# Optimization experiments

Hardware: AMD Instinct MI355X
Metric: run time of the kernel (lower is better)

## Reference

```python
import jax, jax.numpy as jnp
import numpy as np
import math

# config constants (match init_kwargs)
H = 1024; NH = 16; NKV = 4; HD = 64; E = 16; I = 512
NG = 4; TKG = 2; TK = 4; ROUTED_SCALE = 2.5; EPS = 1e-6; THETA = 10000.0
B = 2; S = 1024


def setup_inputs() -> dict:
    key = jax.random.key(0)
    ks = jax.random.split(key, 16)
    sd = 0.02
    inp = {
        "hidden_states": jax.random.normal(ks[0], (B, S, H), jnp.float32),
        "position_ids": jnp.arange(B * S, dtype=jnp.int64).reshape(B, S) % 4096,
        "ln1_w": jnp.ones((H,), jnp.float32),
        "ln2_w": jnp.ones((H,), jnp.float32),
        "q_w": jax.random.normal(ks[1], (NH * HD, H), jnp.float32) * sd,
        "k_w": jax.random.normal(ks[2], (NKV * HD, H), jnp.float32) * sd,
        "v_w": jax.random.normal(ks[3], (NKV * HD, H), jnp.float32) * sd,
        "o_w": jax.random.normal(ks[4], (H, NH * HD), jnp.float32) * sd,
        "gate_w": jax.random.normal(ks[5], (E, H), jnp.float32) * sd,
        "e_bias": jax.random.normal(ks[6], (E,), jnp.float32) * 0.1,
        "W_gu": jax.random.normal(ks[7], (E, 2 * I, H), jnp.float32) * sd,
        "W_d": jax.random.normal(ks[8], (E, H, I), jnp.float32) * sd,
        "sg_w": jax.random.normal(ks[9], (2 * I, H), jnp.float32) * sd,
        "su_w": jax.random.normal(ks[10], (2 * I, H), jnp.float32) * sd,
        "sd_w": jax.random.normal(ks[11], (H, 2 * I), jnp.float32) * sd,
    }
    return inp


def _rmsnorm(x, w, eps=EPS):
    v = jnp.mean(x.astype(jnp.float32) ** 2, axis=-1, keepdims=True)
    return w * (x * jax.lax.rsqrt(v + eps)).astype(w.dtype)


def _rotate_half(x):
    x1, x2 = x[..., : HD // 2], x[..., HD // 2 :]
    return jnp.concatenate([-x2, x1], axis=-1)


def _attention(hs, position_ids, q_w, k_w, v_w, o_w):
    b, s, _ = hs.shape
    q = (hs @ q_w.T).reshape(b, s, NH, HD).transpose(0, 2, 1, 3)   # [B,NH,S,HD]
    k = (hs @ k_w.T).reshape(b, s, NKV, HD).transpose(0, 2, 1, 3)
    v = (hs @ v_w.T).reshape(b, s, NKV, HD).transpose(0, 2, 1, 3)
    # RoPE
    inv_freq = 1.0 / (THETA ** (jnp.arange(0, HD, 2, dtype=jnp.float32) / HD))
    freqs = position_ids.astype(jnp.float32)[..., None] * inv_freq  # [B,S,HD/2]
    emb = jnp.concatenate([freqs, freqs], axis=-1)                  # [B,S,HD]
    cos = jnp.cos(emb)[:, None]                                     # [B,1,S,HD]
    sin = jnp.sin(emb)[:, None]
    q = q * cos + _rotate_half(q) * sin
    k = k * cos + _rotate_half(k) * sin
    # GQA: repeat kv heads
    groups = NH // NKV
    k = jnp.repeat(k, groups, axis=1)
    v = jnp.repeat(v, groups, axis=1)
    scale = 1.0 / math.sqrt(HD)
    scores = jnp.einsum("bhsd,bhtd->bhst", q, k) * scale
    causal = jnp.triu(jnp.full((s, s), -jnp.inf, jnp.float32), k=1)
    scores = scores + causal[None, None]
    attn = jax.nn.softmax(scores.astype(jnp.float32), axis=-1).astype(q.dtype)
    out = jnp.einsum("bhst,bhtd->bhsd", attn, v)
    out = out.transpose(0, 2, 1, 3).reshape(b, s, NH * HD)
    return out @ o_w.T


def _moe(x, gate_w, e_bias, W_gu, W_d, sg_w, su_w, sd_w):
    b, s, h = x.shape
    xf = x.reshape(-1, h)                                     # [T,H]
    T = xf.shape[0]
    logits = xf.astype(jnp.float32) @ gate_w.astype(jnp.float32).T  # [T,E]
    scores = jax.nn.sigmoid(logits)
    sfc = scores + e_bias[None]
    # group-restricted top-k
    gsize = E // NG
    group_scores = sfc.reshape(T, NG, gsize).max(axis=-1)     # [T,NG]
    _, gidx = jax.lax.top_k(group_scores, TKG)                # [T,TKG]
    gmask = jnp.zeros((T, NG), bool).at[jnp.arange(T)[:, None], gidx].set(True)
    smask = jnp.repeat(gmask, gsize, axis=1)                  # [T,E]
    masked = jnp.where(smask, sfc, 0.0)
    _, topk_idx = jax.lax.top_k(masked, TK)                   # [T,TK]
    topk_w = jnp.take_along_axis(scores, topk_idx, axis=1)    # [T,TK]
    topk_w = topk_w / (topk_w.sum(axis=-1, keepdims=True) + 1e-20)
    topk_w = (topk_w * ROUTED_SCALE).astype(xf.dtype)
    # combine weights [T,E] (scatter-add over selected experts)
    combine = jnp.zeros((T, E), xf.dtype).at[
        jnp.arange(T)[:, None], topk_idx].add(topk_w)
    # dense expert compute (static shapes), weighted combine fused in einsum
    gu = jnp.einsum("th,eih->tei", xf, W_gu)                  # [T,E,2I]
    hidden = jax.nn.silu(gu[..., :I]) * gu[..., I:]           # [T,E,I]
    routed = jnp.einsum("tei,ehi,te->th", hidden, W_d, combine)
    # shared experts
    shared = ((jax.nn.silu(xf @ sg_w.T) * (xf @ su_w.T)) @ sd_w.T)
    return (routed + shared).reshape(b, s, h)


def reference(hidden_states, position_ids, ln1_w, ln2_w, q_w, k_w, v_w, o_w,
              gate_w, e_bias, W_gu, W_d, sg_w, su_w, sd_w):
    res = hidden_states
    hs = _rmsnorm(hidden_states, ln1_w)
    hs = res + _attention(hs, position_ids, q_w, k_w, v_w, o_w)
    res = hs
    hs = _rmsnorm(hs, ln2_w)
    hs = res + _moe(hs, gate_w, e_bias, W_gu, W_d, sg_w, su_w, sd_w)
    return hs
```

## Files before the change

### kernel.cpp

```cpp
#include <hip/hip_runtime.h>
#include <hip/hip_bf16.h>
#include <stdint.h>

typedef float f32x4 __attribute__((ext_vector_type(4)));
typedef short s16x8 __attribute__((ext_vector_type(8)));
typedef short s16x4 __attribute__((ext_vector_type(4)));

__device__ __forceinline__ short f2bf(float x) {
    union { float f; uint32_t u; } v; v.f = x;
    uint32_t r = v.u + 0x7fffu + ((v.u >> 16) & 1u);
    return (short)(r >> 16);
}
__device__ __forceinline__ float bf2f(short b) {
    union { uint32_t u; float f; } v; v.u = ((uint32_t)(uint16_t)b) << 16;
    return v.f;
}
__device__ __forceinline__ void gld16(const void* g, void* l) {
    __builtin_amdgcn_global_load_lds((const __attribute__((address_space(1))) uint32_t*)g,
                                     (__attribute__((address_space(3))) uint32_t*)l, 16, 0, 0);
}

__global__ __launch_bounds__(256) void cvt_all_kernel(const float* __restrict__ q, const float* __restrict__ k,
                                                      const float* __restrict__ v, const float* __restrict__ o,
                                                      const float* __restrict__ gu, const float* __restrict__ wd,
                                                      const float* __restrict__ sg, const float* __restrict__ su,
                                                      const float* __restrict__ sd, short* __restrict__ wqkv,
                                                      short* __restrict__ wo, short* __restrict__ wgu,
                                                      short* __restrict__ wdB, short* __restrict__ wsgsu,
                                                      short* __restrict__ wsd) {
    const size_t total = 3866624;
    size_t stride = (size_t)gridDim.x * 256;
    for (size_t i = (size_t)blockIdx.x * 256 + threadIdx.x; i < total; i += stride) {
        const float* src; short* dst;
        if (i < 327680) {
            if (i < 131072) { src = q + i * 8; dst = wqkv + i * 8; }
            else if (i < 163840) { src = k + (i - 131072) * 8; dst = wqkv + 1048576 + (i - 131072) * 8; }
            else if (i < 196608) { src = v + (i - 163840) * 8; dst = wqkv + 1310720 + (i - 163840) * 8; }
            else { src = o + (i - 196608) * 8; dst = wo + (i - 196608) * 8; }
        } else if (i < 3473408) {
            if (i < 2424832) { src = gu + (i - 327680) * 8; dst = wgu + (i - 327680) * 8; }
            else { src = wd + (i - 2424832) * 8; dst = wdB + (i - 2424832) * 8; }
        } else {
            if (i < 3604480) { src = sg + (i - 3473408) * 8; dst = wsgsu + (i - 3473408) * 8; }
            else if (i < 3735552) { src = su + (i - 3604480) * 8; dst = wsgsu + 1048576 + (i - 3604480) * 8; }
            else { src = sd + (i - 3735552) * 8; dst = wsd + (i - 3735552) * 8; }
        }
        f32x4 a = ((const f32x4*)src)[0];
        f32x4 b = ((const f32x4*)src)[1];
        s16x8 o8;
        o8[0] = f2bf(a[0]); o8[1] = f2bf(a[1]); o8[2] = f2bf(a[2]); o8[3] = f2bf(a[3]);
        o8[4] = f2bf(b[0]); o8[5] = f2bf(b[1]); o8[6] = f2bf(b[2]); o8[7] = f2bf(b[3]);
        *(s16x8*)dst = o8;
    }
}

__global__ __launch_bounds__(256) void rmsnorm_kernel(const float* __restrict__ x, const float* __restrict__ w,
                                                      short* __restrict__ out) {
    int t = blockIdx.x;
    f32x4 v = ((const f32x4*)(x + (size_t)t * 1024))[threadIdx.x];
    float ssq = v[0]*v[0] + v[1]*v[1] + v[2]*v[2] + v[3]*v[3];
#pragma unroll
    for (int o = 1; o < 64; o <<= 1) ssq += __shfl_xor(ssq, o);
    __shared__ float red[4];
    if ((threadIdx.x & 63) == 0) red[threadIdx.x >> 6] = ssq;
    __syncthreads();
    float tot = red[0] + red[1] + red[2] + red[3];
    float rs = rsqrtf(tot * (1.0f / 1024.0f) + 1e-6f);
    f32x4 wv = ((const f32x4*)w)[threadIdx.x];
    s16x4 o4;
#pragma unroll
    for (int j = 0; j < 4; ++j) o4[j] = f2bf(v[j] * rs * wv[j]);
    ((s16x4*)(out + (size_t)t * 1024))[threadIdx.x] = o4;
}

__global__ __launch_bounds__(256) void addnorm_kernel(const float* __restrict__ a, const float* __restrict__ b,
                                                      const float* __restrict__ w, float* __restrict__ res,
                                                      short* __restrict__ xf, float* __restrict__ xf32) {
    int t = blockIdx.x;
    f32x4 va = ((const f32x4*)(a + (size_t)t * 1024))[threadIdx.x];
    f32x4 vb = ((const f32x4*)(b + (size_t)t * 1024))[threadIdx.x]
             + ((const f32x4*)(b + (size_t)2048 * 1024 + (size_t)t * 1024))[threadIdx.x];
    f32x4 s = va + vb;
    ((f32x4*)(res + (size_t)t * 1024))[threadIdx.x] = s;
    float ssq = s[0]*s[0] + s[1]*s[1] + s[2]*s[2] + s[3]*s[3];
#pragma unroll
    for (int o = 1; o < 64; o <<= 1) ssq += __shfl_xor(ssq, o);
    __shared__ float red[4];
    if ((threadIdx.x & 63) == 0) red[threadIdx.x >> 6] = ssq;
    __syncthreads();
    float tot = red[0] + red[1] + red[2] + red[3];
    float rs = rsqrtf(tot * (1.0f / 1024.0f) + 1e-6f);
    f32x4 wv = ((const f32x4*)w)[threadIdx.x];
    f32x4 xo;
    s16x4 o4;
#pragma unroll
    for (int j = 0; j < 4; ++j) { xo[j] = s[j] * rs * wv[j]; o4[j] = f2bf(xo[j]); }
    ((f32x4*)(xf32 + (size_t)t * 1024))[threadIdx.x] = xo;
    ((s16x4*)(xf + (size_t)t * 1024))[threadIdx.x] = o4;
}

__global__ __launch_bounds__(256, 4) void gemm2_kernel(const short* __restrict__ A, const short* __restrict__ Bg,
                                                       void* __restrict__ Cv, int M, int N, int Ktot, int Ksub,
                                                       const int* __restrict__ counts, const int* __restrict__ lists,
                                                       const int* __restrict__ plan, int a_shift, int store_bf16) {
    __shared__ short As[2][128 * 32];
    __shared__ short Bs[2][128 * 32];
    int e, bm, bn, k0, Mloc;
    size_t coff;
    const int* rl = nullptr;
    if (plan) {
        int wi = blockIdx.y;
        if (wi >= plan[0]) return;
        int it = plan[1 + wi];
        e = it & 31; bm = (it >> 5) * 128;
        bn = blockIdx.x * 128; k0 = 0;
        Mloc = counts[e]; rl = lists + e * 2048; coff = 0;
    } else {
        e = 0; bm = blockIdx.x * 128; bn = blockIdx.y * 128;
        k0 = blockIdx.z * Ksub; Mloc = M;
        coff = (size_t)blockIdx.z * M * N;
    }
    if (bm >= Mloc) return;
    const short* Bt = Bg + (size_t)e * N * Ktot;
    int tid = threadIdx.x, w = tid >> 6, l = tid & 63;
    int lr = l & 15, lg = l >> 4;
    int rsub = l >> 2, u = l & 3;
    int fs = (rsub & 3) ^ ((rsub >> 2) & 3);
    int colsel = (u ^ fs) * 8;
    int ra = w * 32 + rsub;
    int ga0 = bm + ra;       if (ga0 > Mloc - 1) ga0 = Mloc - 1;
    int ga1 = bm + ra + 16;  if (ga1 > Mloc - 1) ga1 = Mloc - 1;
    int ar0 = rl ? (rl[ga0] >> a_shift) : ga0;
    int ar1 = rl ? (rl[ga1] >> a_shift) : ga1;
    const short* Ap0 = A + (size_t)ar0 * Ktot + k0 + colsel;
    const short* Ap1 = A + (size_t)ar1 * Ktot + k0 + colsel;
    const short* Bp0 = Bt + (size_t)(bn + ra) * Ktot + k0 + colsel;
    const short* Bp1 = Bt + (size_t)(bn + ra + 16) * Ktot + k0 + colsel;
    int lb0 = w * 1024, lb1 = w * 1024 + 512;

    int wm = (w >> 1) * 64, wn = (w & 1) * 64;
    int su = lg ^ (lr & 3) ^ ((lr >> 2) & 3);
    int aoff[4], boff[4];
#pragma unroll
    for (int mf = 0; mf < 4; ++mf) aoff[mf] = (wm + mf * 16 + lr) * 32 + su * 8;
#pragma unroll
    for (int nf = 0; nf < 4; ++nf) boff[nf] = (wn + nf * 16 + lr) * 32 + su * 8;

    f32x4 zero4 = {0.f, 0.f, 0.f, 0.f};
    f32x4 acc[4][4];
#pragma unroll
    for (int mf = 0; mf < 4; ++mf)
#pragma unroll
        for (int nf = 0; nf < 4; ++nf) acc[mf][nf] = zero4;

#define STAGE(buf, kt) do { \
        gld16(Ap0 + (kt) * 32, &As[buf][lb0]); \
        gld16(Ap1 + (kt) * 32, &As[buf][lb1]); \
        gld16(Bp0 + (kt) * 32, &Bs[buf][lb0]); \
        gld16(Bp1 + (kt) * 32, &Bs[buf][lb1]); \
    } while (0)

    int nk = Ksub >> 5;
    STAGE(0, 0);
    asm volatile("s_waitcnt vmcnt(0)");
    __syncthreads();
    for (int kt = 0; kt < nk; ++kt) {
        int cur = kt & 1;
        if (kt + 1 < nk) STAGE(cur ^ 1, kt + 1);
        s16x8 af[4], bfr[4];
#pragma unroll
        for (int mf = 0; mf < 4; ++mf) af[mf] = *(const s16x8*)&As[cur][aoff[mf]];
#pragma unroll
        for (int nf = 0; nf < 4; ++nf) bfr[nf] = *(const s16x8*)&Bs[cur][boff[nf]];
#pragma unroll
        for (int mf = 0; mf < 4; ++mf)
#pragma unroll
            for (int nf = 0; nf < 4; ++nf)
                acc[mf][nf] = __builtin_amdgcn_mfma_f32_16x16x32_bf16(af[mf], bfr[nf], acc[mf][nf], 0, 0, 0);
        __syncthreads();
    }
#undef STAGE
    float* Cf = (float*)Cv;
    short* Cs = (short*)Cv;
#pragma unroll
    for (int mf = 0; mf < 4; ++mf) {
        int rbase = bm + wm + mf * 16 + lg * 4;
#pragma unroll
        for (int r = 0; r < 4; ++r) {
            int grow = rbase + r;
            if (grow < Mloc) {
                int crow = rl ? rl[grow] : grow;
                size_t cb = coff + (size_t)crow * N + bn + wn + lr;
                if (store_bf16) {
#pragma unroll
                    for (int nf = 0; nf < 4; ++nf) Cs[cb + nf * 16] = f2bf(acc[mf][nf][r]);
                } else {
#pragma unroll
                    for (int nf = 0; nf < 4; ++nf) Cf[cb + nf * 16] = acc[mf][nf][r];
                }
            }
        }
    }
}

__global__ __launch_bounds__(64) void rope_kernel(const float* __restrict__ qkv, short* __restrict__ Qr,
                                                  short* __restrict__ Kr, short* __restrict__ Vt) {
    int t = blockIdx.x;
    int b = t >> 10, s = t & 1023;
    int l = threadIdx.x;
    __shared__ float cs[32], sn[32], qrow[1024], krow[256], vrow[256];
    const f32x4* r0 = (const f32x4*)(qkv + (size_t)t * 1536);
    const f32x4* r1 = (const f32x4*)(qkv + (size_t)2048 * 1536 + (size_t)t * 1536);
#pragma unroll
    for (int i = 0; i < 4; ++i) ((f32x4*)qrow)[l + i * 64] = r0[l + i * 64] + r1[l + i * 64];
    ((f32x4*)krow)[l] = r0[256 + l] + r1[256 + l];
    ((f32x4*)vrow)[l] = r0[320 + l] + r1[320 + l];
    if (l < 32) {
        float fr = (float)t * exp2f(-(float)l * 0.41524101186f);
        cs[l] = cosf(fr); sn[l] = sinf(fr);
    }
    __syncthreads();
    int d = l;
    float c = cs[d & 31], sv = sn[d & 31];
#pragma unroll
    for (int h = 0; h < 16; ++h) {
        float x = qrow[h * 64 + d];
        float rot = (d < 32) ? -qrow[h * 64 + d + 32] : qrow[h * 64 + d - 32];
        Qr[((size_t)(b * 16 + h) * 1024 + s) * 64 + d] = f2bf((x * c + rot * sv) * 0.125f);
    }
#pragma unroll
    for (int h = 0; h < 4; ++h) {
        float x = krow[h * 64 + d];
        float rot = (d < 32) ? -krow[h * 64 + d + 32] : krow[h * 64 + d - 32];
        Kr[((size_t)(b * 4 + h) * 1024 + s) * 64 + d] = f2bf(x * c + rot * sv);
        Vt[((size_t)(b * 4 + h) * 64 + d) * 1024 + s] = f2bf(vrow[h * 64 + d]);
    }
}

struct KV { s16x8 k[4]; s16x8 v[4]; };
__device__ __forceinline__ void kv_load(KV& r, const short* Kb, const short* Vb, int k0, int lr, int lg) {
    const short* K0 = Kb + (size_t)(k0 + lr) * 64 + lg * 8;
    const short* K1 = Kb + (size_t)(k0 + 16 + lr) * 64 + lg * 8;
    r.k[0] = *(const s16x8*)K0;
    r.k[1] = *(const s16x8*)(K0 + 32);
    r.k[2] = *(const s16x8*)K1;
    r.k[3] = *(const s16x8*)(K1 + 32);
#pragma unroll
    for (int dt = 0; dt < 4; ++dt)
        r.v[dt] = *(const s16x8*)(Vb + (size_t)(dt * 16 + lr) * 1024 + k0 + lg * 8);
}
__device__ __forceinline__ void chain_step(const KV& kv, s16x8 qf0, s16x8 qf1, f32x4* o,
                                           float& m, float& lsum, short* Pl,
                                           int lr, int lg, int k0, int qmask) {
    f32x4 z = {0.f, 0.f, 0.f, 0.f};
    f32x4 sc0 = z, sc1 = z;
    sc0 = __builtin_amdgcn_mfma_f32_16x16x32_bf16(kv.k[0], qf0, sc0, 0, 0, 0);
    sc0 = __builtin_amdgcn_mfma_f32_16x16x32_bf16(kv.k[1], qf1, sc0, 0, 0, 0);
    sc1 = __builtin_amdgcn_mfma_f32_16x16x32_bf16(kv.k[2], qf0, sc1, 0, 0, 0);
    sc1 = __builtin_amdgcn_mfma_f32_16x16x32_bf16(kv.k[3], qf1, sc1, 0, 0, 0);
#pragma unroll
    for (int r = 0; r < 4; ++r) {
        if (k0 + lg * 4 + r > qmask) sc0[r] = -1e30f;
        if (k0 + 16 + lg * 4 + r > qmask) sc1[r] = -1e30f;
    }
    float tm = fmaxf(fmaxf(fmaxf(sc0[0], sc0[1]), fmaxf(sc0[2], sc0[3])),
                     fmaxf(fmaxf(sc1[0], sc1[1]), fmaxf(sc1[2], sc1[3])));
    tm = fmaxf(tm, __shfl_xor(tm, 16));
    tm = fmaxf(tm, __shfl_xor(tm, 32));
    float newm = fmaxf(m, tm);
    float fac = __expf(m - newm);
    float p[8];
#pragma unroll
    for (int r = 0; r < 4; ++r) { p[r] = __expf(sc0[r] - newm); p[4 + r] = __expf(sc1[r] - newm); }
    float ts = ((p[0] + p[1]) + (p[2] + p[3])) + ((p[4] + p[5]) + (p[6] + p[7]));
    ts += __shfl_xor(ts, 16);
    ts += __shfl_xor(ts, 32);
    lsum = lsum * fac + ts;
    m = newm;
    s16x4 w0, w1;
#pragma unroll
    for (int r = 0; r < 4; ++r) { w0[r] = f2bf(p[r]); w1[r] = f2bf(p[4 + r]); }
    *(s16x4*)&Pl[lr * 40 + lg * 4] = w0;
    *(s16x4*)&Pl[lr * 40 + 16 + lg * 4] = w1;
    s16x8 pf = *(const s16x8*)&Pl[lr * 40 + lg * 8];
#pragma unroll
    for (int dt = 0; dt < 4; ++dt) {
        o[dt] *= fac;
        o[dt] = __builtin_amdgcn_mfma_f32_16x16x32_bf16(kv.v[dt], pf, o[dt], 0, 0, 0);
    }
}

__global__ __launch_bounds__(64) void attn_kernel(const short* __restrict__ Qr, const short* __restrict__ Kr,
                                                  const short* __restrict__ Vt, short* __restrict__ attn_out) {
    int p = blockIdx.x;
    int hb = blockIdx.y;
    int b = hb >> 4, h = hb & 15, kv = h >> 2;
    int l = threadIdx.x;
    int lr = l & 15, lg = l >> 4;
    int q0A = p * 16, q0B = (63 - p) * 16;
    __shared__ short PlA[16 * 40], PlB[16 * 40];
    const short* Qh = Qr + (size_t)(b * 16 + h) * 1024 * 64;
    s16x8 qA0 = *(const s16x8*)(Qh + (size_t)(q0A + lr) * 64 + lg * 8);
    s16x8 qA1 = *(const s16x8*)(Qh + (size_t)(q0A + lr) * 64 + 32 + lg * 8);
    s16x8 qB0 = *(const s16x8*)(Qh + (size_t)(q0B + lr) * 64 + lg * 8);
    s16x8 qB1 = *(const s16x8*)(Qh + (size_t)(q0B + lr) * 64 + 32 + lg * 8);
    const short* Kbase = Kr + (size_t)(b * 4 + kv) * 1024 * 64;
    const short* Vbase = Vt + (size_t)(b * 4 + kv) * 64 * 1024;

    f32x4 zero4 = {0.f, 0.f, 0.f, 0.f};
    f32x4 oA[4], oB[4];
#pragma unroll
    for (int dt = 0; dt < 4; ++dt) { oA[dt] = zero4; oB[dt] = zero4; }
    float mA = -1e30f, lsA = 0.f, mB = -1e30f, lsB = 0.f;
    int ntA = (q0A + 47) >> 5, ntB = (q0B + 47) >> 5;
    int qmA = q0A + lr, qmB = q0B + lr;
    const int BIG = 1 << 29;

    KV b0, b1;
    kv_load(b0, Kbase, Vbase, 0, lr, lg);
    for (int kt = 0; kt < ntB; kt += 2) {
        if (kt + 1 < ntB) kv_load(b1, Kbase, Vbase, (kt + 1) * 32, lr, lg);
        if (kt < ntA) chain_step(b0, qA0, qA1, oA, mA, lsA, PlA, lr, lg, kt * 32,
                                 (kt == ntA - 1) ? qmA : BIG);
        chain_step(b0, qB0, qB1, oB, mB, lsB, PlB, lr, lg, kt * 32,
                   (kt == ntB - 1) ? qmB : BIG);
        if (kt + 1 >= ntB) break;
        if (kt + 2 < ntB) kv_load(b0, Kbase, Vbase, (kt + 2) * 32, lr, lg);
        if (kt + 1 < ntA) chain_step(b1, qA0, qA1, oA, mA, lsA, PlA, lr, lg, (kt + 1) * 32,
                                     (kt + 1 == ntA - 1) ? qmA : BIG);
        chain_step(b1, qB0, qB1, oB, mB, lsB, PlB, lr, lg, (kt + 1) * 32,
                   (kt + 1 == ntB - 1) ? qmB : BIG);
    }
    float invA = 1.f / lsA, invB = 1.f / lsB;
    short* oa = attn_out + ((size_t)(b * 1024 + q0A + lr)) * 1024 + h * 64;
    short* ob = attn_out + ((size_t)(b * 1024 + q0B + lr)) * 1024 + h * 64;
#pragma unroll
    for (int dt = 0; dt < 4; ++dt)
#pragma unroll
        for (int r = 0; r < 4; ++r) {
            oa[dt * 16 + lg * 4 + r] = f2bf(oA[dt][r] * invA);
            ob[dt * 16 + lg * 4 + r] = f2bf(oB[dt][r] * invB);
        }
}

__global__ __launch_bounds__(256) void router_topk_kernel(const float* __restrict__ x32, const float* __restrict__ gw,
                                                          const float* __restrict__ eb, float* __restrict__ tw,
                                                          int* __restrict__ tidx) {
    int t = blockIdx.x * 4 + (threadIdx.x >> 6);
    int l = threadIdx.x & 63;
    const float* x = x32 + (size_t)t * 1024;
    f32x4 xv[4];
#pragma unroll
    for (int j = 0; j < 4; ++j) xv[j] = *(const f32x4*)(x + j * 256 + l * 4);
    float acc[16];
#pragma unroll
    for (int e = 0; e < 16; ++e) {
        float a = 0.f;
#pragma unroll
        for (int j = 0; j < 4; ++j) {
            f32x4 g = *(const f32x4*)(gw + (size_t)e * 1024 + j * 256 + l * 4);
            a += xv[j][0]*g[0] + xv[j][1]*g[1] + xv[j][2]*g[2] + xv[j][3]*g[3];
        }
        acc[e] = a;
    }
#pragma unroll
    for (int e = 0; e < 16; ++e) {
#pragma unroll
        for (int o = 1; o < 64; o <<= 1) acc[e] += __shfl_xor(acc[e], o);
    }
    if (l == 0) {
        float score[16], sfc[16];
#pragma unroll
        for (int e = 0; e < 16; ++e) {
            score[e] = 1.f / (1.f + __expf(-acc[e]));
            sfc[e] = score[e] + eb[e];
        }
        float gs[4];
#pragma unroll
        for (int g = 0; g < 4; ++g)
            gs[g] = fmaxf(fmaxf(sfc[4 * g], sfc[4 * g + 1]), fmaxf(sfc[4 * g + 2], sfc[4 * g + 3]));
        int g1 = 0;
        for (int g = 1; g < 4; ++g) if (gs[g] > gs[g1]) g1 = g;
        int g2 = -1;
        for (int g = 0; g < 4; ++g) {
            if (g == g1) continue;
            if (g2 < 0 || gs[g] > gs[g2]) g2 = g;
        }
        float masked[16];
#pragma unroll
        for (int e = 0; e < 16; ++e) {
            int g = e >> 2;
            masked[e] = (g == g1 || g == g2) ? sfc[e] : 0.0f;
        }
        float tot = 1e-20f;
        int idx[4]; float wv[4];
        for (int k = 0; k < 4; ++k) {
            int bi = 0;
            float bv = -1e30f;
            for (int e2 = 0; e2 < 16; ++e2)
                if (masked[e2] > bv) { bv = masked[e2]; bi = e2; }
            idx[k] = bi;
            wv[k] = score[bi];
            masked[bi] = -1e30f;
            tot += wv[k];
        }
        for (int k = 0; k < 4; ++k) {
            tw[t * 4 + k] = wv[k] / tot * 2.5f;
            tidx[t * 4 + k] = idx[k];
        }
    }
}

__global__ __launch_bounds__(64) void router_lists_kernel(const int* __restrict__ tidx, int* __restrict__ counts,
                                                          int* __restrict__ lists) {
    int e = blockIdx.x;
    int l = threadIdx.x;
    int base = 0;
    for (int it = 0; it < 128; ++it) {
        int p = it * 64 + l;
        bool match = (tidx[p] == e);
        unsigned long long mask = __ballot(match);
        int pos = __popcll(mask & ((1ull << l) - 1ull));
        if (match) lists[e * 2048 + base + pos] = p;
        base += __popcll(mask);
    }
    if (l == 0) counts[e] = base;
}

__global__ void plan_kernel(const int* __restrict__ counts, int* __restrict__ plan) {
    if (threadIdx.x == 0) {
        int n = 0;
        for (int e = 0; e < 16; ++e) {
            int nb = (counts[e] + 127) >> 7;
            for (int m2 = 0; m2 < nb; ++m2) plan[1 + n++] = e | (m2 << 5);
        }
        plan[0] = n;
    }
}

__global__ __launch_bounds__(128) void silu_routed_kernel(const short* __restrict__ gu, short* __restrict__ hid) {
    int pr = blockIdx.x;
    int j = threadIdx.x * 4;
    s16x4 gv = *(const s16x4*)(gu + (size_t)pr * 1024 + j);
    s16x4 uv = *(const s16x4*)(gu + (size_t)pr * 1024 + 512 + j);
    s16x4 o;
#pragma unroll
    for (int k = 0; k < 4; ++k) {
        float gf = bf2f(gv[k]);
        o[k] = f2bf(gf / (1.f + __expf(-gf)) * bf2f(uv[k]));
    }
    *(s16x4*)(hid + (size_t)pr * 512 + j) = o;
}

__global__ __launch_bounds__(256) void silu_shared_kernel(const short* __restrict__ gu, short* __restrict__ h) {
    int t = blockIdx.x;
    int j = threadIdx.x * 4;
    s16x4 gv = *(const s16x4*)(gu + (size_t)t * 2048 + j);
    s16x4 uv = *(const s16x4*)(gu + (size_t)t * 2048 + 1024 + j);
    s16x4 o;
#pragma unroll
    for (int k = 0; k < 4; ++k) {
        float gf = bf2f(gv[k]);
        o[k] = f2bf(gf / (1.f + __expf(-gf)) * bf2f(uv[k]));
    }
    *(s16x4*)(h + (size_t)t * 1024 + j) = o;
}

__global__ __launch_bounds__(256) void combine_kernel(const float* __restrict__ res2, const float* __restrict__ sdp,
                                                      const short* __restrict__ slots, const float* __restrict__ tw,
                                                      float* __restrict__ out) {
    int t = blockIdx.x;
    int i = threadIdx.x;
    f32x4 a = ((const f32x4*)(res2 + (size_t)t * 1024))[i];
    f32x4 s0 = ((const f32x4*)(sdp + (size_t)t * 1024))[i];
    f32x4 s1 = ((const f32x4*)(sdp + (size_t)2048 * 1024 + (size_t)t * 1024))[i];
    f32x4 acc = a + s0 + s1;
#pragma unroll
    for (int s = 0; s < 4; ++s) {
        float w = tw[t * 4 + s];
        s16x4 d = ((const s16x4*)(slots + (size_t)(t * 4 + s) * 1024))[i];
#pragma unroll
        for (int j = 0; j < 4; ++j) acc[j] += bf2f(d[j]) * w;
    }
    ((f32x4*)(out + (size_t)t * 1024))[i] = acc;
}

extern "C" void kernel_launch(void* const* d_in, const int* in_sizes, int n_in,
                              void* d_out, int out_size, void* d_ws, size_t ws_size,
                              hipStream_t stream) {
    const float* hidden = (const float*)d_in[0];
    const float* ln1 = (const float*)d_in[2];
    const float* ln2 = (const float*)d_in[3];
    const float* qw = (const float*)d_in[4];
    const float* kw = (const float*)d_in[5];
    const float* vw = (const float*)d_in[6];
    const float* ow = (const float*)d_in[7];
    const float* gatew = (const float*)d_in[8];
    const float* ebias = (const float*)d_in[9];
    const float* wgu = (const float*)d_in[10];
    const float* wd = (const float*)d_in[11];
    const float* sgw = (const float*)d_in[12];
    const float* suw = (const float*)d_in[13];
    const float* sdw = (const float*)d_in[14];
    float* out = (float*)d_out;

    char* base = (char*)d_ws;
    size_t off = 0;
    auto alloc = [&](size_t bytes) -> char* {
        char* r = base + off;
        off += (bytes + 255) & ~(size_t)255;
        return r;
    };
    const size_t MB = 1u << 20;

    short* wqkv_b = (short*)alloc((size_t)1536 * 1024 * 2);
    short* wo_b   = (short*)alloc((size_t)1024 * 1024 * 2);
    short* wgu_b  = (short*)alloc((size_t)16 * 1024 * 1024 * 2);
    short* wd_b   = (short*)alloc((size_t)16 * 1024 * 512 * 2);
    short* wsgsu_b= (short*)alloc((size_t)2048 * 1024 * 2);
    short* wsd_b  = (short*)alloc((size_t)1024 * 1024 * 2);
    float* res2 = (float*)alloc((size_t)2048 * 1024 * 4);
    short* xf   = (short*)alloc((size_t)2048 * 1024 * 2);
    float* topkw = (float*)alloc(2048 * 4 * 4);
    int* tidx   = (int*)alloc(8192 * 4);
    int* counts = (int*)alloc(64);
    int* lists  = (int*)alloc(16 * 2048 * 4);
    int* plan   = (int*)alloc(512);
    short* gu_or_sgsu = (short*)alloc((size_t)8192 * 1024 * 2);
    short* shhid = (short*)alloc((size_t)2048 * 1024 * 2);
    short* hid   = (short*)alloc((size_t)8192 * 512 * 2);

    char* ov = alloc(50 * MB);
    short* xn1       = (short*)(ov);
    float* qkv_part  = (float*)(ov + 4 * MB);
    short* Qr        = (short*)(ov);
    short* Kr        = (short*)(ov + 28 * MB);
    short* Vt        = (short*)(ov + 29 * MB);
    short* attn_out  = (short*)(ov + 30 * MB);
    float* attnproj_part = (float*)(ov + 34 * MB);
    float* xf32      = (float*)(ov);
    short* down_slot = (short*)(ov + 8 * MB);
    float* sd_part   = (float*)(ov + 24 * MB);

    cvt_all_kernel<<<2048, 256, 0, stream>>>(qw, kw, vw, ow, wgu, wd, sgw, suw, sdw,
                                             wqkv_b, wo_b, wgu_b, wd_b, wsgsu_b, wsd_b);

    rmsnorm_kernel<<<2048, 256, 0, stream>>>(hidden, ln1, xn1);
    gemm2_kernel<<<dim3(16, 12, 2), 256, 0, stream>>>(xn1, wqkv_b, qkv_part, 2048, 1536, 1024, 512,
                                                      nullptr, nullptr, nullptr, 0, 0);
    rope_kernel<<<2048, 64, 0, stream>>>(qkv_part, Qr, Kr, Vt);
    attn_kernel<<<dim3(32, 32, 1), 64, 0, stream>>>(Qr, Kr, Vt, attn_out);
    gemm2_kernel<<<dim3(16, 8, 2), 256, 0, stream>>>(attn_out, wo_b, attnproj_part, 2048, 1024, 1024, 512,
                                                     nullptr, nullptr, nullptr, 0, 0);
    addnorm_kernel<<<2048, 256, 0, stream>>>(hidden, attnproj_part, ln2, res2, xf, xf32);

    router_topk_kernel<<<512, 256, 0, stream>>>(xf32, gatew, ebias, topkw, tidx);
    router_lists_kernel<<<16, 64, 0, stream>>>(tidx, counts, lists);
    plan_kernel<<<1, 64, 0, stream>>>(counts, plan);

    gemm2_kernel<<<dim3(16, 16, 1), 256, 0, stream>>>(xf, wsgsu_b, gu_or_sgsu, 2048, 2048, 1024, 1024,
                                                      nullptr, nullptr, nullptr, 0, 1);
    silu_shared_kernel<<<2048, 256, 0, stream>>>(gu_or_sgsu, shhid);

    gemm2_kernel<<<dim3(8, 80, 1), 256, 0, stream>>>(xf, wgu_b, gu_or_sgsu, 0, 1024, 1024, 1024,
                                                     counts, lists, plan, 2, 1);
    silu_routed_kernel<<<8192, 128, 0, stream>>>(gu_or_sgsu, hid);

    gemm2_kernel<<<dim3(8, 80, 1), 256, 0, stream>>>(hid, wd_b, down_slot, 0, 1024, 512, 512,
                                                     counts, lists, plan, 0, 1);
    gemm2_kernel<<<dim3(16, 8, 2), 256, 0, stream>>>(shhid, wsd_b, sd_part, 2048, 1024, 1024, 512,
                                                     nullptr, nullptr, nullptr, 0, 0);

    combine_kernel<<<2048, 256, 0, stream>>>(res2, sd_part, down_slot, topkw, out);

    (void)in_sizes; (void)n_in; (void)out_size; (void)ws_size;
}
```

Baseline: 297.9 us.

## Deepen split-K to bf16 partials and launch one thread per convert chunk

```diff
diff --git a/kernel.cpp b/kernel.cpp
--- a/kernel.cpp
+++ b/kernel.cpp
@@ -28,30 +28,27 @@
                                                       short* __restrict__ wo, short* __restrict__ wgu,
                                                       short* __restrict__ wdB, short* __restrict__ wsgsu,
                                                       short* __restrict__ wsd) {
-    const size_t total = 3866624;
-    size_t stride = (size_t)gridDim.x * 256;
-    for (size_t i = (size_t)blockIdx.x * 256 + threadIdx.x; i < total; i += stride) {
-        const float* src; short* dst;
-        if (i < 327680) {
-            if (i < 131072) { src = q + i * 8; dst = wqkv + i * 8; }
-            else if (i < 163840) { src = k + (i - 131072) * 8; dst = wqkv + 1048576 + (i - 131072) * 8; }
-            else if (i < 196608) { src = v + (i - 163840) * 8; dst = wqkv + 1310720 + (i - 163840) * 8; }
-            else { src = o + (i - 196608) * 8; dst = wo + (i - 196608) * 8; }
-        } else if (i < 3473408) {
-            if (i < 2424832) { src = gu + (i - 327680) * 8; dst = wgu + (i - 327680) * 8; }
-            else { src = wd + (i - 2424832) * 8; dst = wdB + (i - 2424832) * 8; }
-        } else {
-            if (i < 3604480) { src = sg + (i - 3473408) * 8; dst = wsgsu + (i - 3473408) * 8; }
-            else if (i < 3735552) { src = su + (i - 3604480) * 8; dst = wsgsu + 1048576 + (i - 3604480) * 8; }
-            else { src = sd + (i - 3735552) * 8; dst = wsd + (i - 3735552) * 8; }
-        }
-        f32x4 a = ((const f32x4*)src)[0];
-        f32x4 b = ((const f32x4*)src)[1];
-        s16x8 o8;
-        o8[0] = f2bf(a[0]); o8[1] = f2bf(a[1]); o8[2] = f2bf(a[2]); o8[3] = f2bf(a[3]);
-        o8[4] = f2bf(b[0]); o8[5] = f2bf(b[1]); o8[6] = f2bf(b[2]); o8[7] = f2bf(b[3]);
-        *(s16x8*)dst = o8;
-    }
+    size_t i = (size_t)blockIdx.x * 256 + threadIdx.x;
+    const float* src; short* dst;
+    if (i < 327680) {
+        if (i < 131072) { src = q + i * 8; dst = wqkv + i * 8; }
+        else if (i < 163840) { src = k + (i - 131072) * 8; dst = wqkv + 1048576 + (i - 131072) * 8; }
+        else if (i < 196608) { src = v + (i - 163840) * 8; dst = wqkv + 1310720 + (i - 163840) * 8; }
+        else { src = o + (i - 196608) * 8; dst = wo + (i - 196608) * 8; }
+    } else if (i < 3473408) {
+        if (i < 2424832) { src = gu + (i - 327680) * 8; dst = wgu + (i - 327680) * 8; }
+        else { src = wd + (i - 2424832) * 8; dst = wdB + (i - 2424832) * 8; }
+    } else {
+        if (i < 3604480) { src = sg + (i - 3473408) * 8; dst = wsgsu + (i - 3473408) * 8; }
+        else if (i < 3735552) { src = su + (i - 3604480) * 8; dst = wsgsu + 1048576 + (i - 3604480) * 8; }
+        else { src = sd + (i - 3735552) * 8; dst = wsd + (i - 3735552) * 8; }
+    }
+    f32x4 a = ((const f32x4*)src)[0];
+    f32x4 b = ((const f32x4*)src)[1];
+    s16x8 o8;
+    o8[0] = f2bf(a[0]); o8[1] = f2bf(a[1]); o8[2] = f2bf(a[2]); o8[3] = f2bf(a[3]);
+    o8[4] = f2bf(b[0]); o8[5] = f2bf(b[1]); o8[6] = f2bf(b[2]); o8[7] = f2bf(b[3]);
+    *(s16x8*)dst = o8;
 }
 
 __global__ __launch_bounds__(256) void rmsnorm_kernel(const float* __restrict__ x, const float* __restrict__ w,
@@ -73,13 +70,18 @@
     ((s16x4*)(out + (size_t)t * 1024))[threadIdx.x] = o4;
 }
 
-__global__ __launch_bounds__(256) void addnorm_kernel(const float* __restrict__ a, const float* __restrict__ b,
+__global__ __launch_bounds__(256) void addnorm_kernel(const float* __restrict__ a, const short* __restrict__ b,
                                                       const float* __restrict__ w, float* __restrict__ res,
                                                       short* __restrict__ xf, float* __restrict__ xf32) {
     int t = blockIdx.x;
     f32x4 va = ((const f32x4*)(a + (size_t)t * 1024))[threadIdx.x];
-    f32x4 vb = ((const f32x4*)(b + (size_t)t * 1024))[threadIdx.x]
-             + ((const f32x4*)(b + (size_t)2048 * 1024 + (size_t)t * 1024))[threadIdx.x];
+    f32x4 vb = {0.f, 0.f, 0.f, 0.f};
+#pragma unroll
+    for (int z = 0; z < 4; ++z) {
+        s16x4 dz = *(const s16x4*)(b + (size_t)z * 2048 * 1024 + (size_t)t * 1024 + threadIdx.x * 4);
+#pragma unroll
+        for (int j = 0; j < 4; ++j) vb[j] += bf2f(dz[j]);
+    }
     f32x4 s = va + vb;
     ((f32x4*)(res + (size_t)t * 1024))[threadIdx.x] = s;
     float ssq = s[0]*s[0] + s[1]*s[1] + s[2]*s[2] + s[3]*s[3];
@@ -101,25 +103,26 @@
 
 __global__ __launch_bounds__(256, 4) void gemm2_kernel(const short* __restrict__ A, const short* __restrict__ Bg,
                                                        void* __restrict__ Cv, int M, int N, int Ktot, int Ksub,
+                                                       long long cstride,
                                                        const int* __restrict__ counts, const int* __restrict__ lists,
                                                        const int* __restrict__ plan, int a_shift, int store_bf16) {
     __shared__ short As[2][128 * 32];
     __shared__ short Bs[2][128 * 32];
     int e, bm, bn, k0, Mloc;
-    size_t coff;
+    size_t coff = (size_t)blockIdx.z * cstride;
     const int* rl = nullptr;
     if (plan) {
         int wi = blockIdx.y;
         if (wi >= plan[0]) return;
         int it = plan[1 + wi];
         e = it & 31; bm = (it >> 5) * 128;
-        bn = blockIdx.x * 128; k0 = 0;
-        Mloc = counts[e]; rl = lists + e * 2048; coff = 0;
+        bn = blockIdx.x * 128;
+        Mloc = counts[e]; rl = lists + e * 2048;
     } else {
         e = 0; bm = blockIdx.x * 128; bn = blockIdx.y * 128;
-        k0 = blockIdx.z * Ksub; Mloc = M;
-        coff = (size_t)blockIdx.z * M * N;
-    }
+        Mloc = M;
+    }
+    k0 = blockIdx.z * Ksub;
     if (bm >= Mloc) return;
     const short* Bt = Bg + (size_t)e * N * Ktot;
     int tid = threadIdx.x, w = tid >> 6, l = tid & 63;
@@ -203,18 +206,27 @@
     }
 }
 
-__global__ __launch_bounds__(64) void rope_kernel(const float* __restrict__ qkv, short* __restrict__ Qr,
+__global__ __launch_bounds__(64) void rope_kernel(const short* __restrict__ qkv, short* __restrict__ Qr,
                                                   short* __restrict__ Kr, short* __restrict__ Vt) {
     int t = blockIdx.x;
     int b = t >> 10, s = t & 1023;
     int l = threadIdx.x;
-    __shared__ float cs[32], sn[32], qrow[1024], krow[256], vrow[256];
-    const f32x4* r0 = (const f32x4*)(qkv + (size_t)t * 1536);
-    const f32x4* r1 = (const f32x4*)(qkv + (size_t)2048 * 1536 + (size_t)t * 1536);
-#pragma unroll
-    for (int i = 0; i < 4; ++i) ((f32x4*)qrow)[l + i * 64] = r0[l + i * 64] + r1[l + i * 64];
-    ((f32x4*)krow)[l] = r0[256 + l] + r1[256 + l];
-    ((f32x4*)vrow)[l] = r0[320 + l] + r1[320 + l];
+    __shared__ float cs[32], sn[32], row[1536];
+    float acc[24];
+#pragma unroll
+    for (int c = 0; c < 24; ++c) acc[c] = 0.f;
+#pragma unroll
+    for (int z = 0; z < 4; ++z) {
+        const short* src = qkv + (size_t)z * 2048 * 1536 + (size_t)t * 1536 + l * 24;
+#pragma unroll
+        for (int c8 = 0; c8 < 3; ++c8) {
+            s16x8 v8 = *(const s16x8*)(src + c8 * 8);
+#pragma unroll
+            for (int j = 0; j < 8; ++j) acc[c8 * 8 + j] += bf2f(v8[j]);
+        }
+    }
+#pragma unroll
+    for (int c = 0; c < 24; ++c) row[l * 24 + c] = acc[c];
     if (l < 32) {
         float fr = (float)t * exp2f(-(float)l * 0.41524101186f);
         cs[l] = cosf(fr); sn[l] = sinf(fr);
@@ -224,16 +236,16 @@
     float c = cs[d & 31], sv = sn[d & 31];
 #pragma unroll
     for (int h = 0; h < 16; ++h) {
-        float x = qrow[h * 64 + d];
-        float rot = (d < 32) ? -qrow[h * 64 + d + 32] : qrow[h * 64 + d - 32];
+        float x = row[h * 64 + d];
+        float rot = (d < 32) ? -row[h * 64 + d + 32] : row[h * 64 + d - 32];
         Qr[((size_t)(b * 16 + h) * 1024 + s) * 64 + d] = f2bf((x * c + rot * sv) * 0.125f);
     }
 #pragma unroll
     for (int h = 0; h < 4; ++h) {
-        float x = krow[h * 64 + d];
-        float rot = (d < 32) ? -krow[h * 64 + d + 32] : krow[h * 64 + d - 32];
+        float x = row[1024 + h * 64 + d];
+        float rot = (d < 32) ? -row[1024 + h * 64 + d + 32] : row[1024 + h * 64 + d - 32];
         Kr[((size_t)(b * 4 + h) * 1024 + s) * 64 + d] = f2bf(x * c + rot * sv);
-        Vt[((size_t)(b * 4 + h) * 64 + d) * 1024 + s] = f2bf(vrow[h * 64 + d]);
+        Vt[((size_t)(b * 4 + h) * 64 + d) * 1024 + s] = f2bf(row[1280 + h * 64 + d]);
     }
 }
 
@@ -441,40 +453,51 @@
 __global__ __launch_bounds__(128) void silu_routed_kernel(const short* __restrict__ gu, short* __restrict__ hid) {
     int pr = blockIdx.x;
     int j = threadIdx.x * 4;
-    s16x4 gv = *(const s16x4*)(gu + (size_t)pr * 1024 + j);
-    s16x4 uv = *(const s16x4*)(gu + (size_t)pr * 1024 + 512 + j);
+    float g[4] = {0.f, 0.f, 0.f, 0.f}, u2[4] = {0.f, 0.f, 0.f, 0.f};
+#pragma unroll
+    for (int z = 0; z < 2; ++z) {
+        const short* base = gu + (size_t)z * 8192 * 1024 + (size_t)pr * 1024;
+        s16x4 gz = *(const s16x4*)(base + j);
+        s16x4 uz = *(const s16x4*)(base + 512 + j);
+#pragma unroll
+        for (int k = 0; k < 4; ++k) { g[k] += bf2f(gz[k]); u2[k] += bf2f(uz[k]); }
+    }
     s16x4 o;
 #pragma unroll
-    for (int k = 0; k < 4; ++k) {
-        float gf = bf2f(gv[k]);
-        o[k] = f2bf(gf / (1.f + __expf(-gf)) * bf2f(uv[k]));
-    }
+    for (int k = 0; k < 4; ++k) o[k] = f2bf(g[k] / (1.f + __expf(-g[k])) * u2[k]);
     *(s16x4*)(hid + (size_t)pr * 512 + j) = o;
 }
 
 __global__ __launch_bounds__(256) void silu_shared_kernel(const short* __restrict__ gu, short* __restrict__ h) {
     int t = blockIdx.x;
     int j = threadIdx.x * 4;
-    s16x4 gv = *(const s16x4*)(gu + (size_t)t * 2048 + j);
-    s16x4 uv = *(const s16x4*)(gu + (size_t)t * 2048 + 1024 + j);
+    float g[4] = {0.f, 0.f, 0.f, 0.f}, u2[4] = {0.f, 0.f, 0.f, 0.f};
+#pragma unroll
+    for (int z = 0; z < 2; ++z) {
+        const short* base = gu + (size_t)z * 2048 * 2048 + (size_t)t * 2048;
+        s16x4 gz = *(const s16x4*)(base + j);
+        s16x4 uz = *(const s16x4*)(base + 1024 + j);
+#pragma unroll
+        for (int k = 0; k < 4; ++k) { g[k] += bf2f(gz[k]); u2[k] += bf2f(uz[k]); }
+    }
     s16x4 o;
 #pragma unroll
-    for (int k = 0; k < 4; ++k) {
-        float gf = bf2f(gv[k]);
-        o[k] = f2bf(gf / (1.f + __expf(-gf)) * bf2f(uv[k]));
-    }
+    for (int k = 0; k < 4; ++k) o[k] = f2bf(g[k] / (1.f + __expf(-g[k])) * u2[k]);
     *(s16x4*)(h + (size_t)t * 1024 + j) = o;
 }
 
-__global__ __launch_bounds__(256) void combine_kernel(const float* __restrict__ res2, const float* __restrict__ sdp,
+__global__ __launch_bounds__(256) void combine_kernel(const float* __restrict__ res2, const short* __restrict__ sdp,
                                                       const short* __restrict__ slots, const float* __restrict__ tw,
                                                       float* __restrict__ out) {
     int t = blockIdx.x;
     int i = threadIdx.x;
-    f32x4 a = ((const f32x4*)(res2 + (size_t)t * 1024))[i];
-    f32x4 s0 = ((const f32x4*)(sdp + (size_t)t * 1024))[i];
-    f32x4 s1 = ((const f32x4*)(sdp + (size_t)2048 * 1024 + (size_t)t * 1024))[i];
-    f32x4 acc = a + s0 + s1;
+    f32x4 acc = ((const f32x4*)(res2 + (size_t)t * 1024))[i];
+#pragma unroll
+    for (int z = 0; z < 4; ++z) {
+        s16x4 d = *(const s16x4*)(sdp + (size_t)z * 2048 * 1024 + (size_t)t * 1024 + i * 4);
+#pragma unroll
+        for (int j = 0; j < 4; ++j) acc[j] += bf2f(d[j]);
+    }
 #pragma unroll
     for (int s = 0; s < 4; ++s) {
         float w = tw[t * 4 + s];
@@ -526,50 +549,50 @@
     int* counts = (int*)alloc(64);
     int* lists  = (int*)alloc(16 * 2048 * 4);
     int* plan   = (int*)alloc(512);
-    short* gu_or_sgsu = (short*)alloc((size_t)8192 * 1024 * 2);
     short* shhid = (short*)alloc((size_t)2048 * 1024 * 2);
     short* hid   = (short*)alloc((size_t)8192 * 512 * 2);
 
     char* ov = alloc(50 * MB);
     short* xn1       = (short*)(ov);
-    float* qkv_part  = (float*)(ov + 4 * MB);
+    short* qkv_part  = (short*)(ov + 4 * MB);
     short* Qr        = (short*)(ov);
     short* Kr        = (short*)(ov + 28 * MB);
     short* Vt        = (short*)(ov + 29 * MB);
     short* attn_out  = (short*)(ov + 30 * MB);
-    float* attnproj_part = (float*)(ov + 34 * MB);
+    short* attnproj_part = (short*)(ov + 34 * MB);
     float* xf32      = (float*)(ov);
-    short* down_slot = (short*)(ov + 8 * MB);
-    float* sd_part   = (float*)(ov + 24 * MB);
-
-    cvt_all_kernel<<<2048, 256, 0, stream>>>(qw, kw, vw, ow, wgu, wd, sgw, suw, sdw,
-                                             wqkv_b, wo_b, wgu_b, wd_b, wsgsu_b, wsd_b);
+    short* upbuf     = (short*)(ov);
+    short* down_slot = (short*)(ov);
+    short* sd_part   = (short*)(ov + 16 * MB);
+
+    cvt_all_kernel<<<15104, 256, 0, stream>>>(qw, kw, vw, ow, wgu, wd, sgw, suw, sdw,
+                                              wqkv_b, wo_b, wgu_b, wd_b, wsgsu_b, wsd_b);
 
     rmsnorm_kernel<<<2048, 256, 0, stream>>>(hidden, ln1, xn1);
-    gemm2_kernel<<<dim3(16, 12, 2), 256, 0, stream>>>(xn1, wqkv_b, qkv_part, 2048, 1536, 1024, 512,
-                                                      nullptr, nullptr, nullptr, 0, 0);
+    gemm2_kernel<<<dim3(16, 12, 4), 256, 0, stream>>>(xn1, wqkv_b, qkv_part, 2048, 1536, 1024, 256,
+                                                      2048LL * 1536, nullptr, nullptr, nullptr, 0, 1);
     rope_kernel<<<2048, 64, 0, stream>>>(qkv_part, Qr, Kr, Vt);
     attn_kernel<<<dim3(32, 32, 1), 64, 0, stream>>>(Qr, Kr, Vt, attn_out);
-    gemm2_kernel<<<dim3(16, 8, 2), 256, 0, stream>>>(attn_out, wo_b, attnproj_part, 2048, 1024, 1024, 512,
-                                                     nullptr, nullptr, nullptr, 0, 0);
+    gemm2_kernel<<<dim3(16, 8, 4), 256, 0, stream>>>(attn_out, wo_b, attnproj_part, 2048, 1024, 1024, 256,
+                                                     2048LL * 1024, nullptr, nullptr, nullptr, 0, 1);
     addnorm_kernel<<<2048, 256, 0, stream>>>(hidden, attnproj_part, ln2, res2, xf, xf32);
 
     router_topk_kernel<<<512, 256, 0, stream>>>(xf32, gatew, ebias, topkw, tidx);
     router_lists_kernel<<<16, 64, 0, stream>>>(tidx, counts, lists);
     plan_kernel<<<1, 64, 0, stream>>>(counts, plan);
 
-    gemm2_kernel<<<dim3(16, 16, 1), 256, 0, stream>>>(xf, wsgsu_b, gu_or_sgsu, 2048, 2048, 1024, 1024,
-                                                      nullptr, nullptr, nullptr, 0, 1);
-    silu_shared_kernel<<<2048, 256, 0, stream>>>(gu_or_sgsu, shhid);
-
-    gemm2_kernel<<<dim3(8, 80, 1), 256, 0, stream>>>(xf, wgu_b, gu_or_sgsu, 0, 1024, 1024, 1024,
-                                                     counts, lists, plan, 2, 1);
-    silu_routed_kernel<<<8192, 128, 0, stream>>>(gu_or_sgsu, hid);
+    gemm2_kernel<<<dim3(16, 16, 2), 256, 0, stream>>>(xf, wsgsu_b, upbuf, 2048, 2048, 1024, 512,
+                                                      2048LL * 2048, nullptr, nullptr, nullptr, 0, 1);
+    silu_shared_kernel<<<2048, 256, 0, stream>>>(upbuf, shhid);
+
+    gemm2_kernel<<<dim3(8, 80, 2), 256, 0, stream>>>(xf, wgu_b, upbuf, 0, 1024, 1024, 512,
+                                                     8192LL * 1024, counts, lists, plan, 2, 1);
+    silu_routed_kernel<<<8192, 128, 0, stream>>>(upbuf, hid);
 
     gemm2_kernel<<<dim3(8, 80, 1), 256, 0, stream>>>(hid, wd_b, down_slot, 0, 1024, 512, 512,
-                                                     counts, lists, plan, 0, 1);
-    gemm2_kernel<<<dim3(16, 8, 2), 256, 0, stream>>>(shhid, wsd_b, sd_part, 2048, 1024, 1024, 512,
-                                                     nullptr, nullptr, nullptr, 0, 0);
+                                                     0LL, counts, lists, plan, 0, 1);
+    gemm2_kernel<<<dim3(16, 8, 4), 256, 0, stream>>>(shhid, wsd_b, sd_part, 2048, 1024, 1024, 256,
+                                                     2048LL * 1024, nullptr, nullptr, nullptr, 0, 1);
 
     combine_kernel<<<2048, 256, 0, stream>>>(res2, sd_part, down_slot, topkw, out);
 
```

Measured after the change: 286.0 us. -4.0%, faster.
